# Kernel tuning notes

Measured on AMD Instinct MI355X. Metric: run time of the kernel, lower is better.

Reference implementation:

```python
import jax, jax.numpy as jnp
import numpy as np

D_MODEL = 1024
N_HEADS = 16
D_HEAD = D_MODEL // N_HEADS
ROPE_BASE = 10000.0
B, L = 2, 2048


def setup_inputs() -> dict:
    key = jax.random.key(0)
    k1, k2, k3 = jax.random.split(key, 3)
    x = jax.random.normal(k1, (B, L, D_MODEL), dtype=jnp.float32)
    W_qkv = jax.random.normal(k2, (3 * D_MODEL, D_MODEL), dtype=jnp.float32) * (1.0 / np.sqrt(D_MODEL))
    W_out = jax.random.normal(k3, (D_MODEL, D_MODEL), dtype=jnp.float32) * (1.0 / np.sqrt(D_MODEL))
    position_ids = jnp.broadcast_to(jnp.arange(L, dtype=jnp.int32), (B, L))
    attn_mask_2d = jnp.broadcast_to(jnp.tril(jnp.ones((L, L), dtype=bool)), (B, L, L))
    return {"x": x, "W_qkv": W_qkv, "W_out": W_out,
            "position_ids": position_ids, "attn_mask_2d": attn_mask_2d}


def _apply_rope(t, position_ids, inv_freq):
    # t: (B, H, L, Dh) float32; position_ids: (B, L) int
    f = position_ids.astype(jnp.float32)[:, :, None] * inv_freq  # (B, L, Dh/2)
    cos = jnp.cos(f)[:, None]  # (B, 1, L, Dh/2)
    sin = jnp.sin(f)[:, None]
    x1 = t[..., 0::2]
    x2 = t[..., 1::2]
    rot_even = x1 * cos - x2 * sin
    rot_odd = x1 * sin + x2 * cos
    return jnp.stack((rot_even, rot_odd), axis=-1).reshape(t.shape)


def reference(x, W_qkv, W_out, position_ids, attn_mask_2d):
    Bb, Ll, D = x.shape
    H, Dh = N_HEADS, D // N_HEADS
    inv_freq = 1.0 / (ROPE_BASE ** (jnp.arange(0, Dh, 2, dtype=jnp.float32) / Dh))  # (Dh/2,)
    qkv = jnp.einsum('bld,ed->ble', x, W_qkv).reshape(Bb, Ll, 3, H, Dh)
    qkv = jnp.transpose(qkv, (2, 0, 3, 1, 4))  # (3, B, H, L, Dh)
    q, k, v = qkv[0], qkv[1], qkv[2]
    q = _apply_rope(q.astype(jnp.float32), position_ids, inv_freq).astype(x.dtype)
    k = _apply_rope(k.astype(jnp.float32), position_ids, inv_freq).astype(x.dtype)
    scale = 1.0 / np.sqrt(Dh).astype(np.float32)
    scores = jnp.einsum('bhld,bhmd->bhlm', q, k) * scale  # (B, H, L, L)
    neg = jnp.finfo(scores.dtype).min
    scores = jnp.where(attn_mask_2d[:, None], scores, neg)
    attn = jax.nn.softmax(scores, axis=-1)
    out = jnp.einsum('bhlm,bhmd->bhld', attn, v)
    out = jnp.transpose(out, (0, 2, 1, 3)).reshape(Bb, Ll, D)
    return jnp.einsum('bld,ed->ble', out, W_out)
```

## Files before the change

kernel.cpp:

```cpp
#include <hip/hip_runtime.h>
#include <hip/hip_bf16.h>
#include <math.h>

typedef float f32x4 __attribute__((ext_vector_type(4)));
typedef __bf16 bf16x8 __attribute__((ext_vector_type(8)));

__device__ inline f32x4 mfma16(bf16x8 a, bf16x8 b, f32x4 c) {
    return __builtin_amdgcn_mfma_f32_16x16x32_bf16(a, b, c, 0, 0, 0);
}
__device__ inline unsigned short f2bf(float f) {
    union { float f; unsigned u; } v; v.f = f;
    unsigned r = v.u + 0x7fffu + ((v.u >> 16) & 1u);
    return (unsigned short)(r >> 16);
}
__device__ inline float bf2f(unsigned short b) {
    union { unsigned u; float f; } v; v.u = ((unsigned)b) << 16;
    return v.f;
}
__device__ inline unsigned pack2(float a, float b) {
    return (unsigned)f2bf(a) | ((unsigned)f2bf(b) << 16);
}
__device__ inline f32x4 vzero() { f32x4 z = {0.f, 0.f, 0.f, 0.f}; return z; }

#define GLD16(gptr, lptr)                                                            \
    __builtin_amdgcn_global_load_lds(                                                \
        (const __attribute__((address_space(1))) unsigned int*)(const void*)(gptr),  \
        (__attribute__((address_space(3))) unsigned int*)(void*)(lptr), 16, 0, 0)

__global__ __launch_bounds__(256)
void convert_xw(const float* __restrict__ x, const float* __restrict__ wqkv,
                unsigned short* __restrict__ xb, unsigned short* __restrict__ wqkvb)
{
    int i = blockIdx.x * 256 + threadIdx.x;
    const float* src; unsigned short* dst; int off;
    if (i < 524288) { src = x;    dst = xb;    off = i; }
    else            { src = wqkv; dst = wqkvb; off = i - 524288; }
    const float4* p = (const float4*)src + (size_t)off * 2;
    float4 f0 = p[0], f1 = p[1];
    uint4 o;
    o.x = pack2(f0.x, f0.y); o.y = pack2(f0.z, f0.w);
    o.z = pack2(f1.x, f1.y); o.w = pack2(f1.z, f1.w);
    ((uint4*)dst)[off] = o;
}

template<int MI, int C32, int WPB>
__global__ __launch_bounds__(256, WPB)
void gemm_bt(const unsigned short* __restrict__ A,
             const unsigned short* __restrict__ Wt,
             void* __restrict__ C_, int M, int N, int K)
{
    __shared__ __align__(16) unsigned short As[MI * 32 * 64];
    __shared__ __align__(16) unsigned short Bs[128 * 64];

    const int tid  = threadIdx.x;
    const int wave = tid >> 6;
    const int lane = tid & 63;
    const int quad = lane >> 4;
    const int c0   = lane & 15;
    const int m0 = blockIdx.y * (MI * 32);
    const int n0 = blockIdx.x * 128;
    const int wm = (wave >> 1) * (MI * 16);
    const int wn = (wave & 1) * 64;

    const int lrow   = lane >> 3;
    const int gchunk = (lane & 7) ^ lrow;
    const int goff   = gchunk * 8;

    f32x4 acc[MI][4];
#pragma unroll
    for (int i = 0; i < MI; i++)
#pragma unroll
        for (int j = 0; j < 4; j++) acc[i][j] = vzero();

    for (int k0 = 0; k0 < K; k0 += 64) {
        __syncthreads();
#pragma unroll
        for (int p = 0; p < MI; p++) {
            int r0 = p * 32 + wave * 8;
            GLD16(&A[(size_t)(m0 + r0 + lrow) * K + k0 + goff], &As[r0 * 64]);
        }
#pragma unroll
        for (int p = 0; p < 4; p++) {
            int r0 = p * 32 + wave * 8;
            GLD16(&Wt[(size_t)(n0 + r0 + lrow) * K + k0 + goff], &Bs[r0 * 64]);
        }
        __syncthreads();
#pragma unroll
        for (int kk = 0; kk < 2; kk++) {
            const int pos = ((kk * 4 + quad) ^ (c0 & 7)) * 8;
            bf16x8 af[MI], bfr[4];
#pragma unroll
            for (int i = 0; i < MI; i++)
                af[i] = *(const bf16x8*)&As[(wm + i * 16 + c0) * 64 + pos];
#pragma unroll
            for (int j = 0; j < 4; j++)
                bfr[j] = *(const bf16x8*)&Bs[(wn + j * 16 + c0) * 64 + pos];
#pragma unroll
            for (int i = 0; i < MI; i++)
#pragma unroll
                for (int j = 0; j < 4; j++)
                    acc[i][j] = mfma16(af[i], bfr[j], acc[i][j]);
        }
    }

#pragma unroll
    for (int i = 0; i < MI; i++)
#pragma unroll
        for (int j = 0; j < 4; j++)
#pragma unroll
            for (int r = 0; r < 4; r++) {
                int row  = m0 + wm + i * 16 + quad * 4 + r;
                int colg = n0 + wn + j * 16 + c0;
                if (C32) ((float*)C_)[(size_t)row * N + colg] = acc[i][j][r];
                else ((unsigned short*)C_)[(size_t)row * N + colg] = f2bf(acc[i][j][r]);
            }
}

__global__ __launch_bounds__(256)
void rope_vtrans(const unsigned short* __restrict__ qkv,
                 const int* __restrict__ pos,
                 unsigned short* __restrict__ Qb,
                 unsigned short* __restrict__ Kb,
                 unsigned short* __restrict__ Vt,
                 const float* __restrict__ wout,
                 unsigned short* __restrict__ woutb)
{
    __shared__ unsigned short T[256 * 64];
    const int id = blockIdx.x;
    if (id < 8192) {
        int tid = id * 256 + threadIdx.x;
        int d2 = tid & 31;
        int h  = (tid >> 5) & 15;
        int l  = (tid >> 9) & 2047;
        int b  = tid >> 20;
        size_t row = (size_t)(b * 2048 + l) * 3072;
        int col = h * 64 + 2 * d2;
        float inv_freq = exp2f((float)(-2 * d2) * (13.287712379549449f / 64.0f));
        float f = (float)pos[b * 2048 + l] * inv_freq;
        float s, c;
        sincosf(f, &s, &c);
        unsigned qw = *(const unsigned*)&qkv[row + col];
        unsigned kw = *(const unsigned*)&qkv[row + 1024 + col];
        float q1 = bf2f((unsigned short)qw), q2 = bf2f((unsigned short)(qw >> 16));
        float k1 = bf2f((unsigned short)kw), k2 = bf2f((unsigned short)(kw >> 16));
        const float qs = 0.18033688011112042f;
        size_t o = ((size_t)((b * 16 + h) * 2048 + l)) * 64 + 2 * d2;
        *(unsigned*)&Qb[o] = pack2((q1 * c - q2 * s) * qs, (q1 * s + q2 * c) * qs);
        *(unsigned*)&Kb[o] = pack2(k1 * c - k2 * s, k1 * s + k2 * c);
    } else if (id < 8448) {
        const int id2 = id - 8192;
        const int t = threadIdx.x;
        const int l0 = (id2 & 7) * 256, h = (id2 >> 3) & 15, b = id2 >> 7;
#pragma unroll
        for (int i = 0; i < 8; i++) {
            int c = t + i * 256;
            int r = c >> 3, c8 = c & 7;
            int p = (c8 + (r >> 3)) & 7;
            *(uint4*)&T[r * 64 + p * 8] =
                *(const uint4*)&qkv[(size_t)(b * 2048 + l0 + r) * 3072 + 2048 + h * 64 + c8 * 8];
        }
        __syncthreads();
#pragma unroll
        for (int i = 0; i < 8; i++) {
            int c = t + i * 256;
            int dh = c >> 5, lc = c & 31;
            int blk = dh >> 3;
            unsigned short tmp[8];
#pragma unroll
            for (int j = 0; j < 8; j++) {
                int l = lc * 8 + j;
                int p = (blk + lc) & 7;
                tmp[j] = T[l * 64 + p * 8 + (dh & 7)];
            }
            *(uint4*)&Vt[((size_t)(b * 16 + h) * 64 + dh) * 2048 + l0 + lc * 8] = *(uint4*)tmp;
        }
    } else {
        int i = (id - 8448) * 256 + threadIdx.x;
        const float4* p = (const float4*)wout + (size_t)i * 2;
        float4 f0 = p[0], f1 = p[1];
        uint4 o;
        o.x = pack2(f0.x, f0.y); o.y = pack2(f0.z, f0.w);
        o.z = pack2(f1.x, f1.y); o.w = pack2(f1.z, f1.w);
        ((uint4*)woutb)[i] = o;
    }
}

__global__ __launch_bounds__(256, 4)
void attn(const unsigned short* __restrict__ Q,
          const unsigned short* __restrict__ Kb,
          const unsigned short* __restrict__ Vt,
          unsigned short* __restrict__ O)
{
    __shared__ unsigned short Qs[64 * 64];
    __shared__ unsigned short Ks[64 * 64];
    __shared__ unsigned short Vts[64 * 64];
    __shared__ unsigned short Ps[64 * 64];

    const int tid  = threadIdx.x;
    const int wave = tid >> 6;
    const int lane = tid & 63;
    const int quad = lane >> 4;
    const int c0   = lane & 15;
    const int id = blockIdx.x;
    const int qt = 31 - (id >> 5);
    const int h  = id & 15;
    const int b  = (id >> 4) & 1;
    const size_t headoff = ((size_t)(b * 16 + h)) * 2048 * 64;
    const int q0 = qt * 64;
    const float C = 11.541560327111707f;

    const int ca = tid, cb = tid + 256;
    const int ra = ca >> 3, c8a = ca & 7;
    const int rb = cb >> 3, c8b = cb & 7;
    const int la = ra * 64 + (c8a ^ (ra & 7)) * 8;
    const int lb = rb * 64 + (c8b ^ (rb & 7)) * 8;

    bf16x8 ones;
#pragma unroll
    for (int j = 0; j < 8; j++) ones[j] = (__bf16)1.0f;

    uint4 kreg0, kreg1, vreg0, vreg1;
    {
        kreg0 = *(const uint4*)&Kb[headoff + (size_t)ra * 64 + c8a * 8];
        kreg1 = *(const uint4*)&Kb[headoff + (size_t)rb * 64 + c8b * 8];
        vreg0 = *(const uint4*)&Vt[headoff + (size_t)ra * 2048 + c8a * 8];
        vreg1 = *(const uint4*)&Vt[headoff + (size_t)rb * 2048 + c8b * 8];
    }
    *(uint4*)&Qs[la] = *(const uint4*)&Q[headoff + (size_t)(q0 + ra) * 64 + c8a * 8];
    *(uint4*)&Qs[lb] = *(const uint4*)&Q[headoff + (size_t)(q0 + rb) * 64 + c8b * 8];

    f32x4 o[4];
#pragma unroll
    for (int j = 0; j < 4; j++) o[j] = vzero();
    f32x4 lacc = vzero();

    for (int kt = 0; kt <= qt; kt++) {
        __syncthreads();
        *(uint4*)&Ks[la] = kreg0;
        *(uint4*)&Ks[lb] = kreg1;
        *(uint4*)&Vts[la] = vreg0;
        *(uint4*)&Vts[lb] = vreg1;
        __syncthreads();
        if (kt < qt) {
            size_t k1o = headoff + (size_t)(kt + 1) * 4096;
            kreg0 = *(const uint4*)&Kb[k1o + (size_t)ra * 64 + c8a * 8];
            kreg1 = *(const uint4*)&Kb[k1o + (size_t)rb * 64 + c8b * 8];
            vreg0 = *(const uint4*)&Vt[headoff + (size_t)ra * 2048 + (kt + 1) * 64 + c8a * 8];
            vreg1 = *(const uint4*)&Vt[headoff + (size_t)rb * 2048 + (kt + 1) * 64 + c8b * 8];
        }

        f32x4 s[4];
#pragma unroll
        for (int nj = 0; nj < 4; nj++) s[nj] = vzero();
#pragma unroll
        for (int kk = 0; kk < 2; kk++) {
            const int pos = ((kk * 4 + quad) ^ (c0 & 7)) * 8;
            bf16x8 aq = *(const bf16x8*)&Qs[(wave * 16 + c0) * 64 + pos];
#pragma unroll
            for (int nj = 0; nj < 4; nj++) {
                bf16x8 bk = *(const bf16x8*)&Ks[(nj * 16 + c0) * 64 + pos];
                s[nj] = mfma16(aq, bk, s[nj]);
            }
        }
        if (kt == qt) {
#pragma unroll
            for (int nj = 0; nj < 4; nj++)
#pragma unroll
                for (int r = 0; r < 4; r++) {
                    int key  = nj * 16 + c0;
                    int qrow = wave * 16 + quad * 4 + r;
                    if (key > qrow) s[nj][r] = -1e38f;
                }
        }
#pragma unroll
        for (int nj = 0; nj < 4; nj++)
#pragma unroll
            for (int r = 0; r < 4; r++) {
                union { float f; unsigned u; } pv;
                pv.f = __builtin_amdgcn_exp2f(s[nj][r] - C);
                int row = wave * 16 + quad * 4 + r;
                int col = nj * 16 + c0;
                int pp = ((col >> 3) + row) & 7;
                Ps[row * 64 + pp * 8 + (col & 7)] = (unsigned short)(pv.u >> 16);
            }
        __syncthreads();
#pragma unroll
        for (int kk = 0; kk < 2; kk++) {
            const int pos = ((kk * 4 + quad) ^ (c0 & 7)) * 8;
            int prow = wave * 16 + c0;
            int pp = ((kk * 4 + quad) + prow) & 7;
            bf16x8 ap = *(const bf16x8*)&Ps[prow * 64 + pp * 8];
            lacc = mfma16(ap, ones, lacc);
#pragma unroll
            for (int cj = 0; cj < 4; cj++) {
                bf16x8 bv = *(const bf16x8*)&Vts[(cj * 16 + c0) * 64 + pos];
                o[cj] = mfma16(ap, bv, o[cj]);
            }
        }
    }

#pragma unroll
    for (int r = 0; r < 4; r++) {
        float inv = 1.0f / lacc[r];
        int ql = q0 + wave * 16 + quad * 4 + r;
        size_t base = ((size_t)b * 2048 + ql) * 1024 + h * 64;
#pragma unroll
        for (int cj = 0; cj < 4; cj++)
            O[base + cj * 16 + c0] = f2bf(o[cj][r] * inv);
    }
}

extern "C" void kernel_launch(void* const* d_in, const int* in_sizes, int n_in,
                              void* d_out, int out_size, void* d_ws, size_t ws_size,
                              hipStream_t stream) {
    const int* pos = (const int*)d_in[3];

    unsigned short* regA = (unsigned short*)d_ws;
    unsigned short* regB = regA + (size_t)4096 * 1024;
    unsigned short* regC = regB + (size_t)4096 * 1024;
    unsigned short* regD = regC + (size_t)4096 * 1024;
    unsigned short* regE = regD + (size_t)4096 * 3072;

    unsigned short* xb    = regA;
    unsigned short* wqkvb = regB;
    unsigned short* qkv   = regD;
    unsigned short* Qb    = regA;
    unsigned short* Kb    = regB;
    unsigned short* Vt    = regC;
    unsigned short* Ob    = regD;
    unsigned short* woutb = regE;

    convert_xw<<<3584, 256, 0, stream>>>((const float*)d_in[0], (const float*)d_in[1],
                                         xb, wqkvb);
    gemm_bt<4, 0, 4><<<dim3(24, 32), 256, 0, stream>>>(xb, wqkvb, qkv, 4096, 3072, 1024);
    rope_vtrans<<<8960, 256, 0, stream>>>(qkv, pos, Qb, Kb, Vt,
                                          (const float*)d_in[2], woutb);
    attn<<<1024, 256, 0, stream>>>(Qb, Kb, Vt, Ob);
    gemm_bt<2, 1, 3><<<dim3(8, 64), 256, 0, stream>>>(Ob, woutb, d_out, 4096, 1024, 1024);
}
```

Baseline: 196.1 us.

## Fuse RoPE and head-major scatter into QKV GEMM epilogue

Adds a dedicated QKV GEMM whose epilogue applies RoPE and the query scale to Q and K, and writes Q, K and V straight into head-major layouts. It uses a lane shuffle to fetch the paired element and a swizzled block order over M tiles. The separate RoPE pass over the bf16 qkv buffer goes away, leaving a smaller V-transpose plus W_out conversion kernel. The cost is per-element sincos in the epilogue and scattered 2-byte stores, and workspace buffers are reassigned.

```diff
diff --git a/kernel.cpp b/kernel.cpp
--- a/kernel.cpp
+++ b/kernel.cpp
@@ -43,6 +43,109 @@
     ((uint4*)dst)[off] = o;
 }
 
+__global__ __launch_bounds__(256, 4)
+void gemm_qkv(const unsigned short* __restrict__ A,
+              const unsigned short* __restrict__ Wt,
+              const int* __restrict__ pos,
+              unsigned short* __restrict__ Qb,
+              unsigned short* __restrict__ Kb,
+              unsigned short* __restrict__ Vb)
+{
+    __shared__ __align__(16) unsigned short As[128 * 64];
+    __shared__ __align__(16) unsigned short Bs[128 * 64];
+
+    const int tid  = threadIdx.x;
+    const int wave = tid >> 6;
+    const int lane = tid & 63;
+    const int quad = lane >> 4;
+    const int c0   = lane & 15;
+    const int lin  = blockIdx.x;
+    const int m0 = (((lin & 7) << 2) | ((lin >> 3) & 3)) * 128;
+    const int n0 = (lin >> 5) * 128;
+    const int wm = (wave >> 1) * 64;
+    const int wn = (wave & 1) * 64;
+    const int K = 1024;
+
+    const int lrow   = lane >> 3;
+    const int gchunk = (lane & 7) ^ lrow;
+    const int goff   = gchunk * 8;
+
+    f32x4 acc[4][4];
+#pragma unroll
+    for (int i = 0; i < 4; i++)
+#pragma unroll
+        for (int j = 0; j < 4; j++) acc[i][j] = vzero();
+
+    for (int k0 = 0; k0 < K; k0 += 64) {
+        __syncthreads();
+#pragma unroll
+        for (int p = 0; p < 4; p++) {
+            int r0 = p * 32 + wave * 8;
+            GLD16(&A[(size_t)(m0 + r0 + lrow) * K + k0 + goff], &As[r0 * 64]);
+            GLD16(&Wt[(size_t)(n0 + r0 + lrow) * K + k0 + goff], &Bs[r0 * 64]);
+        }
+        __syncthreads();
+#pragma unroll
+        for (int kk = 0; kk < 2; kk++) {
+            const int pos8 = ((kk * 4 + quad) ^ (c0 & 7)) * 8;
+            bf16x8 af[4], bfr[4];
+#pragma unroll
+            for (int i = 0; i < 4; i++)
+                af[i] = *(const bf16x8*)&As[(wm + i * 16 + c0) * 64 + pos8];
+#pragma unroll
+            for (int j = 0; j < 4; j++)
+                bfr[j] = *(const bf16x8*)&Bs[(wn + j * 16 + c0) * 64 + pos8];
+#pragma unroll
+            for (int i = 0; i < 4; i++)
+#pragma unroll
+                for (int j = 0; j < 4; j++)
+                    acc[i][j] = mfma16(af[i], bfr[j], acc[i][j]);
+        }
+    }
+
+    const int sel = n0 < 1024 ? 0 : (n0 < 2048 ? 1 : 2);
+    if (sel == 2) {
+#pragma unroll
+        for (int i = 0; i < 4; i++)
+#pragma unroll
+            for (int j = 0; j < 4; j++) {
+                int n = n0 + wn + j * 16 + c0 - 2048;
+                int h = n >> 6, d = n & 63;
+#pragma unroll
+                for (int r = 0; r < 4; r++) {
+                    int row = m0 + wm + i * 16 + quad * 4 + r;
+                    int b = row >> 11, l = row & 2047;
+                    Vb[((size_t)(b * 16 + h) * 2048 + l) * 64 + d] = f2bf(acc[i][j][r]);
+                }
+            }
+    } else {
+        unsigned short* dst = sel ? Kb : Qb;
+        const int nbase = sel ? 1024 : 0;
+        const float qs = sel ? 1.0f : 0.18033688011112042f;
+#pragma unroll
+        for (int j = 0; j < 4; j++) {
+            int n = n0 + wn + j * 16 + c0 - nbase;
+            int h = n >> 6, d = n & 63;
+            float invf = exp2f((float)(-2 * (d >> 1)) * (13.287712379549449f / 64.0f));
+            float sgnsel = (lane & 1) ? 1.0f : -1.0f;
+#pragma unroll
+            for (int i = 0; i < 4; i++)
+#pragma unroll
+                for (int r = 0; r < 4; r++) {
+                    int row = m0 + wm + i * 16 + quad * 4 + r;
+                    int b = row >> 11, l = row & 2047;
+                    float f = (float)pos[b * 2048 + l] * invf;
+                    float s, c;
+                    sincosf(f, &s, &c);
+                    float x  = acc[i][j][r];
+                    float xp = __shfl_xor(x, 1, 64);
+                    float out = (x * c + xp * (sgnsel * s)) * qs;
+                    dst[((size_t)(b * 16 + h) * 2048 + l) * 64 + d] = f2bf(out);
+                }
+        }
+    }
+}
+
 template<int MI, int C32, int WPB>
 __global__ __launch_bounds__(256, WPB)
 void gemm_bt(const unsigned short* __restrict__ A,
@@ -117,47 +220,22 @@
 }
 
 __global__ __launch_bounds__(256)
-void rope_vtrans(const unsigned short* __restrict__ qkv,
-                 const int* __restrict__ pos,
-                 unsigned short* __restrict__ Qb,
-                 unsigned short* __restrict__ Kb,
-                 unsigned short* __restrict__ Vt,
-                 const float* __restrict__ wout,
-                 unsigned short* __restrict__ woutb)
+void vtrans_wout(const unsigned short* __restrict__ Vb, unsigned short* __restrict__ Vt,
+                 const float* __restrict__ wout, unsigned short* __restrict__ woutb)
 {
     __shared__ unsigned short T[256 * 64];
     const int id = blockIdx.x;
-    if (id < 8192) {
-        int tid = id * 256 + threadIdx.x;
-        int d2 = tid & 31;
-        int h  = (tid >> 5) & 15;
-        int l  = (tid >> 9) & 2047;
-        int b  = tid >> 20;
-        size_t row = (size_t)(b * 2048 + l) * 3072;
-        int col = h * 64 + 2 * d2;
-        float inv_freq = exp2f((float)(-2 * d2) * (13.287712379549449f / 64.0f));
-        float f = (float)pos[b * 2048 + l] * inv_freq;
-        float s, c;
-        sincosf(f, &s, &c);
-        unsigned qw = *(const unsigned*)&qkv[row + col];
-        unsigned kw = *(const unsigned*)&qkv[row + 1024 + col];
-        float q1 = bf2f((unsigned short)qw), q2 = bf2f((unsigned short)(qw >> 16));
-        float k1 = bf2f((unsigned short)kw), k2 = bf2f((unsigned short)(kw >> 16));
-        const float qs = 0.18033688011112042f;
-        size_t o = ((size_t)((b * 16 + h) * 2048 + l)) * 64 + 2 * d2;
-        *(unsigned*)&Qb[o] = pack2((q1 * c - q2 * s) * qs, (q1 * s + q2 * c) * qs);
-        *(unsigned*)&Kb[o] = pack2(k1 * c - k2 * s, k1 * s + k2 * c);
-    } else if (id < 8448) {
-        const int id2 = id - 8192;
+    if (id < 256) {
         const int t = threadIdx.x;
-        const int l0 = (id2 & 7) * 256, h = (id2 >> 3) & 15, b = id2 >> 7;
+        const int l0 = (id & 7) * 256, h = (id >> 3) & 15, b = id >> 7;
+        const size_t base = ((size_t)(b * 16 + h)) * 2048;
 #pragma unroll
         for (int i = 0; i < 8; i++) {
             int c = t + i * 256;
             int r = c >> 3, c8 = c & 7;
             int p = (c8 + (r >> 3)) & 7;
             *(uint4*)&T[r * 64 + p * 8] =
-                *(const uint4*)&qkv[(size_t)(b * 2048 + l0 + r) * 3072 + 2048 + h * 64 + c8 * 8];
+                *(const uint4*)&Vb[(base + l0 + r) * 64 + c8 * 8];
         }
         __syncthreads();
 #pragma unroll
@@ -172,10 +250,10 @@
                 int p = (blk + lc) & 7;
                 tmp[j] = T[l * 64 + p * 8 + (dh & 7)];
             }
-            *(uint4*)&Vt[((size_t)(b * 16 + h) * 64 + dh) * 2048 + l0 + lc * 8] = *(uint4*)tmp;
+            *(uint4*)&Vt[(base * 64) + (size_t)dh * 2048 + l0 + lc * 8] = *(uint4*)tmp;
         }
     } else {
-        int i = (id - 8448) * 256 + threadIdx.x;
+        int i = (id - 256) * 256 + threadIdx.x;
         const float4* p = (const float4*)wout + (size_t)i * 2;
         float4 f0 = p[0], f1 = p[1];
         uint4 o;
@@ -323,18 +401,20 @@
 
     unsigned short* xb    = regA;
     unsigned short* wqkvb = regB;
-    unsigned short* qkv   = regD;
     unsigned short* Qb    = regA;
-    unsigned short* Kb    = regB;
+    unsigned short* Qb_safe = regD + (size_t)4096 * 1024;
+    unsigned short* Kb    = regB + 0;
+    unsigned short* Kb_safe = regD + (size_t)4096 * 2048;
+    unsigned short* Vb    = regD;
     unsigned short* Vt    = regC;
-    unsigned short* Ob    = regD;
+    unsigned short* Ob    = regA;
     unsigned short* woutb = regE;
+    (void)Qb; (void)Kb;
 
     convert_xw<<<3584, 256, 0, stream>>>((const float*)d_in[0], (const float*)d_in[1],
                                          xb, wqkvb);
-    gemm_bt<4, 0, 4><<<dim3(24, 32), 256, 0, stream>>>(xb, wqkvb, qkv, 4096, 3072, 1024);
-    rope_vtrans<<<8960, 256, 0, stream>>>(qkv, pos, Qb, Kb, Vt,
-                                          (const float*)d_in[2], woutb);
-    attn<<<1024, 256, 0, stream>>>(Qb, Kb, Vt, Ob);
+    gemm_qkv<<<768, 256, 0, stream>>>(xb, wqkvb, pos, Qb_safe, Kb_safe, Vb);
+    vtrans_wout<<<768, 256, 0, stream>>>(Vb, Vt, (const float*)d_in[2], woutb);
+    attn<<<1024, 256, 0, stream>>>(Qb_safe, Kb_safe, Vt, Ob);
     gemm_bt<2, 1, 3><<<dim3(8, 64), 256, 0, stream>>>(Ob, woutb, d_out, 4096, 1024, 1024);
 }
```

New measurement: 389.3 us. +98.5%, slower.

## Pair short and long causal query tiles per attention block to balance work

Applied to the files above, without the earlier changes.

Each attention block now handles two query tiles, qt=jp and qt=31-jp, for the same head. The K/V tiles loaded for the long tile are shared with the short one, so every block does equal work and the grid drops from 1024 to 512 blocks. This is meant to remove the causal load imbalance and reuse the K/V loads across both tiles. In exchange it doubles Q/P shared memory, adds registers for a second set of accumulators, lowers the occupancy hint from 4 to 2, and halves the number of blocks.

```diff
diff --git a/kernel.cpp b/kernel.cpp
--- a/kernel.cpp
+++ b/kernel.cpp
@@ -185,16 +185,18 @@
     }
 }
 
-__global__ __launch_bounds__(256, 4)
+__global__ __launch_bounds__(256, 2)
 void attn(const unsigned short* __restrict__ Q,
           const unsigned short* __restrict__ Kb,
           const unsigned short* __restrict__ Vt,
           unsigned short* __restrict__ O)
 {
-    __shared__ unsigned short Qs[64 * 64];
+    __shared__ unsigned short QsA[64 * 64];
+    __shared__ unsigned short QsB[64 * 64];
     __shared__ unsigned short Ks[64 * 64];
     __shared__ unsigned short Vts[64 * 64];
-    __shared__ unsigned short Ps[64 * 64];
+    __shared__ unsigned short PsA[64 * 64];
+    __shared__ unsigned short PsB[64 * 64];
 
     const int tid  = threadIdx.x;
     const int wave = tid >> 6;
@@ -202,16 +204,17 @@
     const int quad = lane >> 4;
     const int c0   = lane & 15;
     const int id = blockIdx.x;
-    const int qt = 31 - (id >> 5);
+    const int jp = id >> 5;
     const int h  = id & 15;
     const int b  = (id >> 4) & 1;
+    const int qtA = jp, qtB = 31 - jp;
     const size_t headoff = ((size_t)(b * 16 + h)) * 2048 * 64;
-    const int q0 = qt * 64;
+    const int q0A = qtA * 64, q0B = qtB * 64;
     const float C = 11.541560327111707f;
 
-    const int ca = tid, cb = tid + 256;
+    const int ca = tid, cb2 = tid + 256;
     const int ra = ca >> 3, c8a = ca & 7;
-    const int rb = cb >> 3, c8b = cb & 7;
+    const int rb = cb2 >> 3, c8b = cb2 & 7;
     const int la = ra * 64 + (c8a ^ (ra & 7)) * 8;
     const int lb = rb * 64 + (c8b ^ (rb & 7)) * 8;
 
@@ -226,87 +229,149 @@
         vreg0 = *(const uint4*)&Vt[headoff + (size_t)ra * 2048 + c8a * 8];
         vreg1 = *(const uint4*)&Vt[headoff + (size_t)rb * 2048 + c8b * 8];
     }
-    *(uint4*)&Qs[la] = *(const uint4*)&Q[headoff + (size_t)(q0 + ra) * 64 + c8a * 8];
-    *(uint4*)&Qs[lb] = *(const uint4*)&Q[headoff + (size_t)(q0 + rb) * 64 + c8b * 8];
-
-    f32x4 o[4];
-#pragma unroll
-    for (int j = 0; j < 4; j++) o[j] = vzero();
-    f32x4 lacc = vzero();
-
-    for (int kt = 0; kt <= qt; kt++) {
+    *(uint4*)&QsA[la] = *(const uint4*)&Q[headoff + (size_t)(q0A + ra) * 64 + c8a * 8];
+    *(uint4*)&QsA[lb] = *(const uint4*)&Q[headoff + (size_t)(q0A + rb) * 64 + c8b * 8];
+    *(uint4*)&QsB[la] = *(const uint4*)&Q[headoff + (size_t)(q0B + ra) * 64 + c8a * 8];
+    *(uint4*)&QsB[lb] = *(const uint4*)&Q[headoff + (size_t)(q0B + rb) * 64 + c8b * 8];
+
+    f32x4 oA[4], oB[4];
+#pragma unroll
+    for (int j = 0; j < 4; j++) { oA[j] = vzero(); oB[j] = vzero(); }
+    f32x4 laccA = vzero(), laccB = vzero();
+
+    for (int kt = 0; kt <= qtB; kt++) {
         __syncthreads();
         *(uint4*)&Ks[la] = kreg0;
         *(uint4*)&Ks[lb] = kreg1;
         *(uint4*)&Vts[la] = vreg0;
         *(uint4*)&Vts[lb] = vreg1;
         __syncthreads();
-        if (kt < qt) {
+        if (kt < qtB) {
             size_t k1o = headoff + (size_t)(kt + 1) * 4096;
             kreg0 = *(const uint4*)&Kb[k1o + (size_t)ra * 64 + c8a * 8];
             kreg1 = *(const uint4*)&Kb[k1o + (size_t)rb * 64 + c8b * 8];
             vreg0 = *(const uint4*)&Vt[headoff + (size_t)ra * 2048 + (kt + 1) * 64 + c8a * 8];
             vreg1 = *(const uint4*)&Vt[headoff + (size_t)rb * 2048 + (kt + 1) * 64 + c8b * 8];
         }
-
-        f32x4 s[4];
-#pragma unroll
-        for (int nj = 0; nj < 4; nj++) s[nj] = vzero();
-#pragma unroll
-        for (int kk = 0; kk < 2; kk++) {
-            const int pos = ((kk * 4 + quad) ^ (c0 & 7)) * 8;
-            bf16x8 aq = *(const bf16x8*)&Qs[(wave * 16 + c0) * 64 + pos];
-#pragma unroll
-            for (int nj = 0; nj < 4; nj++) {
-                bf16x8 bk = *(const bf16x8*)&Ks[(nj * 16 + c0) * 64 + pos];
-                s[nj] = mfma16(aq, bk, s[nj]);
-            }
-        }
-        if (kt == qt) {
+        const bool doA = (kt <= qtA);
+
+        {
+            f32x4 s[4];
+#pragma unroll
+            for (int nj = 0; nj < 4; nj++) s[nj] = vzero();
+#pragma unroll
+            for (int kk = 0; kk < 2; kk++) {
+                const int pos = ((kk * 4 + quad) ^ (c0 & 7)) * 8;
+                bf16x8 aq = *(const bf16x8*)&QsB[(wave * 16 + c0) * 64 + pos];
+#pragma unroll
+                for (int nj = 0; nj < 4; nj++) {
+                    bf16x8 bk = *(const bf16x8*)&Ks[(nj * 16 + c0) * 64 + pos];
+                    s[nj] = mfma16(aq, bk, s[nj]);
+                }
+            }
+            if (kt == qtB) {
+#pragma unroll
+                for (int nj = 0; nj < 4; nj++)
+#pragma unroll
+                    for (int r = 0; r < 4; r++) {
+                        int key  = nj * 16 + c0;
+                        int qrow = wave * 16 + quad * 4 + r;
+                        if (key > qrow) s[nj][r] = -1e38f;
+                    }
+            }
 #pragma unroll
             for (int nj = 0; nj < 4; nj++)
 #pragma unroll
                 for (int r = 0; r < 4; r++) {
-                    int key  = nj * 16 + c0;
-                    int qrow = wave * 16 + quad * 4 + r;
-                    if (key > qrow) s[nj][r] = -1e38f;
+                    union { float f; unsigned u; } pv;
+                    pv.f = __builtin_amdgcn_exp2f(s[nj][r] - C);
+                    int row = wave * 16 + quad * 4 + r;
+                    int col = nj * 16 + c0;
+                    int pp = ((col >> 3) + row) & 7;
+                    PsB[row * 64 + pp * 8 + (col & 7)] = (unsigned short)(pv.u >> 16);
                 }
         }
-#pragma unroll
-        for (int nj = 0; nj < 4; nj++)
-#pragma unroll
-            for (int r = 0; r < 4; r++) {
-                union { float f; unsigned u; } pv;
-                pv.f = __builtin_amdgcn_exp2f(s[nj][r] - C);
-                int row = wave * 16 + quad * 4 + r;
-                int col = nj * 16 + c0;
-                int pp = ((col >> 3) + row) & 7;
-                Ps[row * 64 + pp * 8 + (col & 7)] = (unsigned short)(pv.u >> 16);
-            }
-        __syncthreads();
+        if (doA) {
+            f32x4 s[4];
+#pragma unroll
+            for (int nj = 0; nj < 4; nj++) s[nj] = vzero();
+#pragma unroll
+            for (int kk = 0; kk < 2; kk++) {
+                const int pos = ((kk * 4 + quad) ^ (c0 & 7)) * 8;
+                bf16x8 aq = *(const bf16x8*)&QsA[(wave * 16 + c0) * 64 + pos];
+#pragma unroll
+                for (int nj = 0; nj < 4; nj++) {
+                    bf16x8 bk = *(const bf16x8*)&Ks[(nj * 16 + c0) * 64 + pos];
+                    s[nj] = mfma16(aq, bk, s[nj]);
+                }
+            }
+            if (kt == qtA) {
+#pragma unroll
+                for (int nj = 0; nj < 4; nj++)
+#pragma unroll
+                    for (int r = 0; r < 4; r++) {
+                        int key  = nj * 16 + c0;
+                        int qrow = wave * 16 + quad * 4 + r;
+                        if (key > qrow) s[nj][r] = -1e38f;
+                    }
+            }
+#pragma unroll
+            for (int nj = 0; nj < 4; nj++)
+#pragma unroll
+                for (int r = 0; r < 4; r++) {
+                    union { float f; unsigned u; } pv;
+                    pv.f = __builtin_amdgcn_exp2f(s[nj][r] - C);
+                    int row = wave * 16 + quad * 4 + r;
+                    int col = nj * 16 + c0;
+                    int pp = ((col >> 3) + row) & 7;
+                    PsA[row * 64 + pp * 8 + (col & 7)] = (unsigned short)(pv.u >> 16);
+                }
+        }
+        __syncthreads();
+
 #pragma unroll
         for (int kk = 0; kk < 2; kk++) {
             const int pos = ((kk * 4 + quad) ^ (c0 & 7)) * 8;
             int prow = wave * 16 + c0;
             int pp = ((kk * 4 + quad) + prow) & 7;
-            bf16x8 ap = *(const bf16x8*)&Ps[prow * 64 + pp * 8];
-            lacc = mfma16(ap, ones, lacc);
+            bf16x8 ap = *(const bf16x8*)&PsB[prow * 64 + pp * 8];
+            laccB = mfma16(ap, ones, laccB);
 #pragma unroll
             for (int cj = 0; cj < 4; cj++) {
                 bf16x8 bv = *(const bf16x8*)&Vts[(cj * 16 + c0) * 64 + pos];
-                o[cj] = mfma16(ap, bv, o[cj]);
+                oB[cj] = mfma16(ap, bv, oB[cj]);
+            }
+        }
+        if (doA) {
+#pragma unroll
+            for (int kk = 0; kk < 2; kk++) {
+                const int pos = ((kk * 4 + quad) ^ (c0 & 7)) * 8;
+                int prow = wave * 16 + c0;
+                int pp = ((kk * 4 + quad) + prow) & 7;
+                bf16x8 ap = *(const bf16x8*)&PsA[prow * 64 + pp * 8];
+                laccA = mfma16(ap, ones, laccA);
+#pragma unroll
+                for (int cj = 0; cj < 4; cj++) {
+                    bf16x8 bv = *(const bf16x8*)&Vts[(cj * 16 + c0) * 64 + pos];
+                    oA[cj] = mfma16(ap, bv, oA[cj]);
+                }
             }
         }
     }
 
 #pragma unroll
     for (int r = 0; r < 4; r++) {
-        float inv = 1.0f / lacc[r];
-        int ql = q0 + wave * 16 + quad * 4 + r;
-        size_t base = ((size_t)b * 2048 + ql) * 1024 + h * 64;
-#pragma unroll
-        for (int cj = 0; cj < 4; cj++)
-            O[base + cj * 16 + c0] = f2bf(o[cj][r] * inv);
+        float invA = 1.0f / laccA[r];
+        float invB = 1.0f / laccB[r];
+        int qlA = q0A + wave * 16 + quad * 4 + r;
+        int qlB = q0B + wave * 16 + quad * 4 + r;
+        size_t baseA = ((size_t)b * 2048 + qlA) * 1024 + h * 64;
+        size_t baseB = ((size_t)b * 2048 + qlB) * 1024 + h * 64;
+#pragma unroll
+        for (int cj = 0; cj < 4; cj++) {
+            O[baseA + cj * 16 + c0] = f2bf(oA[cj][r] * invA);
+            O[baseB + cj * 16 + c0] = f2bf(oB[cj][r] * invB);
+        }
     }
 }
 
@@ -335,6 +400,6 @@
     gemm_bt<4, 0, 4><<<dim3(24, 32), 256, 0, stream>>>(xb, wqkvb, qkv, 4096, 3072, 1024);
     rope_vtrans<<<8960, 256, 0, stream>>>(qkv, pos, Qb, Kb, Vt,
                                           (const float*)d_in[2], woutb);
-    attn<<<1024, 256, 0, stream>>>(Qb, Kb, Vt, Ob);
+    attn<<<512, 256, 0, stream>>>(Qb, Kb, Vt, Ob);
     gemm_bt<2, 1, 3><<<dim3(8, 64), 256, 0, stream>>>(Ob, woutb, d_out, 4096, 1024, 1024);
 }
```

Measured after the change: 194.0 us. About the same (-1.0%).
